# Optimization experiments

Measured on AMD Instinct MI355X. Metric: run time of the kernel, lower is better.

The kernel has to match this reference:

```python
import jax, jax.numpy as jnp
import numpy as np

B, L, D = 16, 196, 512
M = 4096            # existing memory slots
DIS_MEM_LEN = 4096  # M+1 > DIS_MEM_LEN -> eviction always triggers (static shapes)


def setup_inputs() -> dict:
    key = jax.random.key(0)
    ks = jax.random.split(key, 10)
    x = jax.random.normal(ks[0], (B, L, D), jnp.float32)
    feat_mem = jax.random.normal(ks[1], (B, M, D), jnp.float32)
    # freq >= 6 so rm_mask = (freq > 5) is guaranteed nonempty (matches torch
    # branch `if rm_mask.sum() > 0`) and asserts freq != 0, min <= freq hold.
    freq_mem = 6 + jax.random.randint(ks[2], (B, M), 0, 50, jnp.int32)
    min_mem = jax.random.randint(ks[3], (B, M), 0, 6, jnp.int32)
    s = float(1.0 / np.sqrt(D))
    Wv = jax.random.uniform(ks[4], (D, D), jnp.float32, -s, s)
    bv = jax.random.uniform(ks[5], (D,), jnp.float32, -s, s)
    Wu = jax.random.uniform(ks[6], (D, D), jnp.float32, -s, s)
    bu = jax.random.uniform(ks[7], (D,), jnp.float32, -s, s)
    Ww = jax.random.uniform(ks[8], (D, 1), jnp.float32, -s, s)
    bw = jax.random.uniform(ks[9], (1,), jnp.float32, -s, s)
    return dict(x=x, feat_mem=feat_mem, freq_mem=freq_mem, min_mem=min_mem,
                Wv=Wv, bv=bv, Wu=Wu, bu=bu, Ww=Ww, bw=bw)


def reference(x, feat_mem, freq_mem, min_mem, Wv, bv, Wu, bu, Ww, bw):
    bs = x.shape[0]
    cls = x[:, :1, :]                                  # [B, 1, D]
    feat = jnp.concatenate([feat_mem, cls], axis=1)    # [B, M+1, D]
    zero = jnp.zeros((bs, 1), jnp.int32)
    freq = jnp.concatenate([freq_mem, zero], axis=1)   # [B, M+1]
    mn = jnp.concatenate([min_mem, zero], axis=1)      # [B, M+1]

    # gated attention score: sigmoid(Linear(tanh(Lv x) * sigmoid(Lu x)))
    attn_v = jnp.tanh(feat @ Wv + bv)
    attn_u = jax.nn.sigmoid(feat @ Wu + bu)
    attn_score = jax.nn.sigmoid((attn_v * attn_u) @ Ww + bw)  # [B, M+1, 1]

    # eval-mode cur_iter_mask = ones; feat is detached in z in the original
    z = jnp.sum(attn_score * jax.lax.stop_gradient(feat), axis=1)  # [B, D]

    # update_freq_mem: mask is all ones -> +1 everywhere
    freq = freq + 1
    # update_min_mem: argmin of attn_score along memory dim, scatter +1
    attn_idx = jnp.argmin(attn_score[..., 0], axis=1)  # [B]
    mn = mn.at[jnp.arange(bs), attn_idx].add(1)

    # eviction: M+1 > dis_mem_len, remove argmax(min/freq * (freq>5)) per batch
    rm_mask = freq > 5
    ratio = mn.astype(jnp.float32) / freq.astype(jnp.float32) * rm_mask
    rm_idx = jnp.argmax(ratio, axis=1)                 # [B]
    col = jnp.arange(freq.shape[1])[None, :]
    is_rm = col == rm_idx[:, None]                     # [B, M+1] one True per row
    # stable argsort puts kept indices first (in original order), removed one last
    order = jnp.argsort(is_rm, axis=1, stable=True)[:, : freq.shape[1] - 1]
    feat_out = jnp.take_along_axis(feat, order[..., None], axis=1)  # [B, M, D]
    freq_out = jnp.take_along_axis(freq, order, axis=1)             # [B, M]
    min_out = jnp.take_along_axis(mn, order, axis=1)                # [B, M]
    return z, feat_out, freq_out, min_out
```

## Files before the change

kernel.cpp:

```cpp
#include <hip/hip_runtime.h>
#include <cmath>

#define NB 16
#define MM 4096
#define MP1 4097
#define DD 512
#define LSEQ 196
#define NRB 65
#define PSH (32 * 16 * 512)
#define MARGIN 0.05f
#define CANDMAX 128

typedef float f32x4 __attribute__((ext_vector_type(4)));
typedef short bf16x8 __attribute__((ext_vector_type(8)));
typedef unsigned short u16x8 __attribute__((ext_vector_type(8)));

static __device__ __forceinline__ unsigned short bf16_rne(float x) {
  union { float f; unsigned u; } c; c.f = x;
  unsigned u = c.u;
  u += 0x7fffu + ((u >> 16) & 1u);
  return (unsigned short)(u >> 16);
}
static __device__ __forceinline__ float sig_prec(float v) { return 1.0f / (1.0f + expf(-v)); }
static __device__ __forceinline__ float sig_fast(float v) { return 1.0f / (1.0f + __expf(-v)); }
static __device__ __forceinline__ float tanh_fast(float v) { return fmaf(2.0f, sig_fast(2.0f * v), -1.0f); }

__global__ __launch_bounds__(256) void k_packW(const float* __restrict__ Wv,
                                               const float* __restrict__ Wu,
                                               unsigned short* __restrict__ Bp) {
  const int gid = blockIdx.x * 256 + threadIdx.x;
  const int l = gid & 63;
  const int ksg = (gid >> 6) & 15;
  const int ctg = (gid >> 10) & 31;
  const int mat = gid >> 15;
  const float* W = mat ? Wu : Wv;
  const int col = ctg * 16 + (l & 15);
  const int kb = ksg * 32 + (l >> 4) * 8;
  u16x8 hi;
#pragma unroll
  for (int i = 0; i < 8; ++i) hi[i] = bf16_rne(W[(size_t)(kb + i) * DD + col]);
  *(u16x8*)(Bp + (size_t)mat * PSH + ((size_t)(ctg * 16 + ksg)) * 512 + l * 8) = hi;
}

__global__ __launch_bounds__(256) void k_packA(const float* __restrict__ x,
                                               const float* __restrict__ feat_mem,
                                               unsigned short* __restrict__ Ah) {
  const int b = blockIdx.y, rb = blockIdx.x;
  const int kc = threadIdx.x >> 6, l = threadIdx.x & 63;
  unsigned short* dst = Ah + (((size_t)b * NRB + rb) * 4 + kc) * 8192;
#pragma unroll
  for (int f = 0; f < 16; ++f) {
    const int ks = f >> 2, rt = f & 3;
    const int grow = rb * 64 + rt * 16 + (l & 15);
    const int k = kc * 128 + ks * 32 + (l >> 4) * 8;
    float v[8] = {0.f, 0.f, 0.f, 0.f, 0.f, 0.f, 0.f, 0.f};
    if (grow <= MM) {
      const float* src = (grow < MM) ? feat_mem + ((size_t)b * MM + grow) * DD + k
                                     : x + (size_t)b * LSEQ * DD + k;
      const float4 t0 = ((const float4*)src)[0];
      const float4 t1 = ((const float4*)src)[1];
      v[0] = t0.x; v[1] = t0.y; v[2] = t0.z; v[3] = t0.w;
      v[4] = t1.x; v[5] = t1.y; v[6] = t1.z; v[7] = t1.w;
    }
    u16x8 hi;
#pragma unroll
    for (int i = 0; i < 8; ++i) hi[i] = bf16_rne(v[i]);
    *(u16x8*)(dst + f * 512 + l * 8) = hi;
  }
}

__global__ __launch_bounds__(256, 3) void k_scores(
    const unsigned short* __restrict__ Ah, const unsigned short* __restrict__ Bp,
    const float* __restrict__ bv, const float* __restrict__ bu,
    const float* __restrict__ Ww, float* __restrict__ logits) {
  const int rb = blockIdx.x, colb = blockIdx.y, b = blockIdx.z;
  const int tid = threadIdx.x, wave = tid >> 6, l = tid & 63;
  __shared__ __align__(16) unsigned short Alds[2][8192];
  __shared__ float sred[4][64];

  const unsigned short* Abase = Ah + (((size_t)b * NRB + rb) * 4) * 8192;

  f32x4 accv[4][2], accu[4][2];
#pragma unroll
  for (int i = 0; i < 4; ++i)
#pragma unroll
    for (int j = 0; j < 2; ++j) {
      accv[i][j] = (f32x4){0.f, 0.f, 0.f, 0.f};
      accu[i][j] = (f32x4){0.f, 0.f, 0.f, 0.f};
    }

#define STAGE(kc, buf)                                                              \
  {                                                                                 \
    _Pragma("unroll")                                                               \
    for (int r = 0; r < 4; ++r) {                                                   \
      const unsigned short* g = Abase + (kc) * 8192 + r * 2048 + tid * 8;           \
      __builtin_amdgcn_global_load_lds(                                             \
          (const __attribute__((address_space(1))) void*)g,                         \
          (__attribute__((address_space(3))) void*)&Alds[(buf)][r * 2048 + tid * 8],\
          16, 0, 0);                                                                \
    }                                                                               \
  }

  STAGE(0, 0);
  __syncthreads();
  for (int kc = 0; kc < 4; ++kc) {
    if (kc < 3) STAGE(kc + 1, (kc + 1) & 1);
    const unsigned short* Ab = Alds[kc & 1];
#pragma unroll
    for (int ks = 0; ks < 4; ++ks) {
      bf16x8 hiA[4];
#pragma unroll
      for (int rt = 0; rt < 4; ++rt)
        hiA[rt] = *(const bf16x8*)(Ab + (ks * 4 + rt) * 512 + l * 8);
      const int ksg = kc * 4 + ks;
#pragma unroll
      for (int ct = 0; ct < 2; ++ct) {
        const int ctg = colb * 8 + wave * 2 + ct;
        const unsigned short* fb = Bp + ((size_t)(ctg * 16 + ksg)) * 512 + l * 8;
        const bf16x8 hv = *(const bf16x8*)fb;
        const bf16x8 hu = *(const bf16x8*)(fb + PSH);
#pragma unroll
        for (int rt = 0; rt < 4; ++rt) {
          accv[rt][ct] = __builtin_amdgcn_mfma_f32_16x16x32_bf16(hiA[rt], hv, accv[rt][ct], 0, 0, 0);
          accu[rt][ct] = __builtin_amdgcn_mfma_f32_16x16x32_bf16(hiA[rt], hu, accu[rt][ct], 0, 0, 0);
        }
      }
    }
    __syncthreads();
  }
#undef STAGE

  float prow[4][4];
#pragma unroll
  for (int i = 0; i < 4; ++i)
#pragma unroll
    for (int j = 0; j < 4; ++j) prow[i][j] = 0.f;
#pragma unroll
  for (int ct = 0; ct < 2; ++ct) {
    const int col = colb * 128 + wave * 32 + ct * 16 + (l & 15);
    const float bvc = bv[col], buc = bu[col], wwc = Ww[col];
#pragma unroll
    for (int rt = 0; rt < 4; ++rt)
#pragma unroll
      for (int r = 0; r < 4; ++r) {
        const float vv = tanh_fast(accv[rt][ct][r] + bvc);
        const float uu = sig_fast(accu[rt][ct][r] + buc);
        prow[rt][r] = fmaf(vv * uu, wwc, prow[rt][r]);
      }
  }
#pragma unroll
  for (int off = 1; off < 16; off <<= 1)
#pragma unroll
    for (int rt = 0; rt < 4; ++rt)
#pragma unroll
      for (int r = 0; r < 4; ++r) prow[rt][r] += __shfl_xor(prow[rt][r], off, 64);

  if ((l & 15) == 0) {
#pragma unroll
    for (int rt = 0; rt < 4; ++rt)
#pragma unroll
      for (int r = 0; r < 4; ++r) sred[wave][rt * 16 + (l >> 4) * 4 + r] = prow[rt][r];
  }
  __syncthreads();
  if (tid < 64) {
    const float s = sred[0][tid] + sred[1][tid] + sred[2][tid] + sred[3][tid];
    const int row = rb * 64 + tid;
    if (row < MP1) atomicAdd(&logits[(size_t)b * MP1 + row], s);
  }
}

__global__ __launch_bounds__(256) void k_z(const float* __restrict__ x,
                                           const float* __restrict__ feat_mem,
                                           const float* __restrict__ logits,
                                           const float* __restrict__ bw,
                                           float* __restrict__ zacc) {
  const int b = blockIdx.y;
  const int rc = blockIdx.x >> 2;
  const int dc = blockIdx.x & 3;
  const int t = threadIdx.x;
  const int rpar = t >> 5;
  const int d = dc * 128 + (t & 31) * 4;
  const int rbeg = rc * 512;
  const int rend = (rc == 7) ? MP1 : rc * 512 + 512;
  const float bw0 = bw[0];
  float4 acc = make_float4(0.f, 0.f, 0.f, 0.f);
  for (int r = rbeg + rpar; r < rend; r += 8) {
    const float s = sig_fast(logits[(size_t)b * MP1 + r] + bw0);
    const float* src = (r < MM) ? feat_mem + ((size_t)b * MM + r) * DD
                                : x + (size_t)b * LSEQ * DD;
    const float4 f = *(const float4*)(src + d);
    acc.x = fmaf(s, f.x, acc.x);
    acc.y = fmaf(s, f.y, acc.y);
    acc.z = fmaf(s, f.z, acc.z);
    acc.w = fmaf(s, f.w, acc.w);
  }
  __shared__ float4 red[256];
  red[t] = acc;
  __syncthreads();
  if (t < 32) {
    float4 s = red[t];
#pragma unroll
    for (int j = 1; j < 8; ++j) {
      const float4 o = red[t + 32 * j];
      s.x += o.x; s.y += o.y; s.z += o.z; s.w += o.w;
    }
    atomicAdd(&zacc[(size_t)b * DD + d + 0], s.x);
    atomicAdd(&zacc[(size_t)b * DD + d + 1], s.y);
    atomicAdd(&zacc[(size_t)b * DD + d + 2], s.z);
    atomicAdd(&zacc[(size_t)b * DD + d + 3], s.w);
  }
}

__global__ __launch_bounds__(256) void k_cand(const float* __restrict__ logits,
                                              int* __restrict__ cand,
                                              int* __restrict__ cnt) {
  const int b = blockIdx.x, tid = threadIdx.x;
  __shared__ float sv[256];
  __shared__ int scnt;
  float m = INFINITY;
  for (int i = tid; i < MP1; i += 256) m = fminf(m, logits[(size_t)b * MP1 + i]);
  sv[tid] = m;
  __syncthreads();
  for (int s = 128; s >= 1; s >>= 1) {
    if (tid < s) sv[tid] = fminf(sv[tid], sv[tid + s]);
    __syncthreads();
  }
  const float minv = sv[0];
  if (tid == 0) scnt = 0;
  __syncthreads();
  for (int i = tid; i < MP1; i += 256) {
    if (logits[(size_t)b * MP1 + i] <= minv + MARGIN) {
      const int p = atomicAdd(&scnt, 1);
      if (p < CANDMAX) cand[b * CANDMAX + p] = i;
    }
  }
  __syncthreads();
  if (tid == 0) cnt[b] = (scnt < CANDMAX) ? scnt : CANDMAX;
}

__global__ __launch_bounds__(256) void k_refine(
    const float* __restrict__ x, const float* __restrict__ feat_mem,
    const float* __restrict__ Wv, const float* __restrict__ bv,
    const float* __restrict__ Wu, const float* __restrict__ bu,
    const float* __restrict__ Ww,
    const int* __restrict__ cand, const int* __restrict__ cnt,
    float* __restrict__ candpart) {
  const int b = blockIdx.z, c = blockIdx.y, cb = blockIdx.x;
  if (c >= cnt[b]) return;
  const int row = cand[b * CANDMAX + c];
  const int tid = threadIdx.x;
  const int jl = tid & 63;
  const int ks = tid >> 6;
  const int col = cb * 64 + jl;
  __shared__ __align__(16) float sfeat[DD];
  __shared__ float sredv[4][64];
  __shared__ float sredu[4][64];
  const float* src = (row < MM) ? feat_mem + ((size_t)b * MM + row) * DD
                                : x + (size_t)b * LSEQ * DD;
  if (tid < 128) ((float4*)sfeat)[tid] = ((const float4*)src)[tid];
  __syncthreads();
  float v = 0.f, u = 0.f;
  const float* wvp = Wv + (size_t)(ks * 128) * DD + col;
  const float* wup = Wu + (size_t)(ks * 128) * DD + col;
#pragma unroll 8
  for (int k = 0; k < 128; ++k) {
    const float a = sfeat[ks * 128 + k];
    v = fmaf(a, wvp[(size_t)k * DD], v);
    u = fmaf(a, wup[(size_t)k * DD], u);
  }
  sredv[ks][jl] = v;
  sredu[ks][jl] = u;
  __syncthreads();
  if (tid < 64) {
    const float vv = (sredv[0][jl] + sredv[1][jl]) + (sredv[2][jl] + sredv[3][jl]);
    const float uu = (sredu[0][jl] + sredu[1][jl]) + (sredu[2][jl] + sredu[3][jl]);
    float g = tanhf(vv + bv[col]) * sig_prec(uu + bu[col]) * Ww[col];
#pragma unroll
    for (int off = 1; off < 64; off <<= 1) g += __shfl_xor(g, off, 64);
    if (jl == 0) candpart[((size_t)b * CANDMAX + c) * 8 + cb] = g;
  }
}

__global__ __launch_bounds__(256) void k_finalize2(
    const int* __restrict__ cand, const float* __restrict__ candpart,
    const int* __restrict__ cnt, const int* __restrict__ freq_mem,
    const int* __restrict__ min_mem, const float* __restrict__ zacc,
    float* __restrict__ out_z, float* __restrict__ out_freq,
    float* __restrict__ out_min, int* __restrict__ rm_attn) {
  const int b = blockIdx.x, tid = threadIdx.x;
  __shared__ float sv[256];
  __shared__ int si[256];
  __shared__ int sn[256], sd[256], sj[256];
  __shared__ int s_attn, s_rm;

  const int n = cnt[b];
  float v = INFINITY;
  int idx = MP1;
  if (tid < n) {
    const float* p = candpart + ((size_t)b * CANDMAX + tid) * 8;
    v = ((p[0] + p[1]) + (p[2] + p[3])) + ((p[4] + p[5]) + (p[6] + p[7]));
    idx = cand[b * CANDMAX + tid];
  }
  sv[tid] = v; si[tid] = idx;
  __syncthreads();
  for (int s = 128; s >= 1; s >>= 1) {
    if (tid < s) {
      const float v2 = sv[tid + s]; const int i2 = si[tid + s];
      if (v2 < sv[tid] || (v2 == sv[tid] && i2 < si[tid])) { sv[tid] = v2; si[tid] = i2; }
    }
    __syncthreads();
  }
  if (tid == 0) s_attn = si[0];
  __syncthreads();
  const int attn = s_attn;

  int bn = -1, bd = 1, bj = 0;
  for (int i = tid; i < MP1; i += 256) {
    int num, den;
    if (i < MM) {
      den = freq_mem[(size_t)b * MM + i] + 1;
      num = min_mem[(size_t)b * MM + i] + (i == attn ? 1 : 0);
      if (den <= 5) num = 0;
    } else { den = 1; num = 0; }
    if (num * bd > bn * den) { bn = num; bd = den; bj = i; }
  }
  sn[tid] = bn; sd[tid] = bd; sj[tid] = bj;
  __syncthreads();
  for (int s = 128; s >= 1; s >>= 1) {
    if (tid < s) {
      const int n2 = sn[tid + s], d2 = sd[tid + s], j2 = sj[tid + s];
      const int lft = n2 * sd[tid], rgt = sn[tid] * d2;
      if (lft > rgt || (lft == rgt && j2 < sj[tid])) { sn[tid] = n2; sd[tid] = d2; sj[tid] = j2; }
    }
    __syncthreads();
  }
  if (tid == 0) { s_rm = sj[0]; rm_attn[b * 2] = attn; rm_attn[b * 2 + 1] = sj[0]; }
  __syncthreads();
  const int rm = s_rm;

  for (int i = tid; i < MM; i += 256) {
    const int src = (i < rm) ? i : i + 1;
    int fv, mv;
    if (src < MM) {
      fv = freq_mem[(size_t)b * MM + src] + 1;
      mv = min_mem[(size_t)b * MM + src] + (src == attn ? 1 : 0);
    } else {
      fv = 1; mv = (attn == MM) ? 1 : 0;
    }
    out_freq[(size_t)b * MM + i] = (float)fv;
    out_min[(size_t)b * MM + i] = (float)mv;
  }
  for (int d = tid; d < DD; d += 256) out_z[(size_t)b * DD + d] = zacc[(size_t)b * DD + d];
}

__global__ __launch_bounds__(256) void k_gather(
    const float* __restrict__ feat_mem, const float* __restrict__ x,
    const int* __restrict__ rm_attn, float* __restrict__ out_feat) {
  const int b = blockIdx.y;
  const int rm = rm_attn[b * 2 + 1];
  const int row = blockIdx.x * 4 + (threadIdx.x >> 6);
  const int lane = threadIdx.x & 63;
  const int src = (row < rm) ? row : row + 1;
  const float* sp = (src < MM) ? (feat_mem + ((size_t)b * MM + src) * DD)
                               : (x + (size_t)b * LSEQ * DD);
  float* dp = out_feat + ((size_t)b * MM + row) * DD;
  const float4 v0 = reinterpret_cast<const float4*>(sp)[lane];
  const float4 v1 = reinterpret_cast<const float4*>(sp)[lane + 64];
  reinterpret_cast<float4*>(dp)[lane] = v0;
  reinterpret_cast<float4*>(dp)[lane + 64] = v1;
}

extern "C" void kernel_launch(void* const* d_in, const int* in_sizes, int n_in,
                              void* d_out, int out_size, void* d_ws, size_t ws_size,
                              hipStream_t stream) {
  const float* x        = (const float*)d_in[0];
  const float* feat_mem = (const float*)d_in[1];
  const int*   freq_mem = (const int*)d_in[2];
  const int*   min_mem  = (const int*)d_in[3];
  const float* Wv       = (const float*)d_in[4];
  const float* bv       = (const float*)d_in[5];
  const float* Wu       = (const float*)d_in[6];
  const float* bu       = (const float*)d_in[7];
  const float* Ww       = (const float*)d_in[8];
  const float* bw       = (const float*)d_in[9];

  float* ws       = (float*)d_ws;
  float* logits   = ws;
  float* zacc     = ws + NB * MP1;
  float* candpart = zacc + NB * DD;
  int*   cand     = (int*)(candpart + NB * CANDMAX * 8);
  int*   cnt      = cand + NB * CANDMAX;
  int*   rm_attn  = cnt + NB;
  unsigned short* Bp = (unsigned short*)(rm_attn + 32);

  float* out_z    = (float*)d_out;
  float* out_feat = out_z + NB * DD;
  float* out_freq = out_feat + (size_t)NB * MM * DD;
  float* out_min  = out_freq + (size_t)NB * MM;

  unsigned short* Ah = (unsigned short*)out_feat;

  hipMemsetAsync(logits, 0, (NB * MP1 + NB * DD) * sizeof(float), stream);
  hipMemsetAsync(cnt, 0, NB * sizeof(int), stream);

  k_packW<<<dim3(256), dim3(256), 0, stream>>>(Wv, Wu, Bp);
  k_packA<<<dim3(NRB, NB), dim3(256), 0, stream>>>(x, feat_mem, Ah);
  k_scores<<<dim3(NRB, 4, NB), dim3(256), 0, stream>>>(Ah, Bp, bv, bu, Ww, logits);
  k_z<<<dim3(32, NB), dim3(256), 0, stream>>>(x, feat_mem, logits, bw, zacc);
  k_cand<<<dim3(NB), dim3(256), 0, stream>>>(logits, cand, cnt);
  k_refine<<<dim3(8, CANDMAX, NB), dim3(256), 0, stream>>>(x, feat_mem, Wv, bv, Wu, bu, Ww,
                                                           cand, cnt, candpart);
  k_finalize2<<<dim3(NB), dim3(256), 0, stream>>>(cand, candpart, cnt, freq_mem, min_mem, zacc,
                                                  out_z, out_freq, out_min, rm_attn);
  k_gather<<<dim3(MM / 4, NB), dim3(256), 0, stream>>>(feat_mem, x, rm_attn, out_feat);
}
```

Measured before the change: 263.3 us.

## Fuse fp32-to-bf16 activation packing into the scores GEMM kernel

Removes the separate k_packA pass that converted feat_mem to a bf16 staging buffer. The scores kernel now loads fp32 rows directly, converts them with packed bf16 conversion instructions, and writes them into double-buffered LDS while the MFMAs for the previous K chunk run. Blocks grow to 512 threads covering 256 output columns, and Wv/Wu tiles are interleaved so each wave reads consecutive tiles. This avoids writing and re-reading the bf16 copy of the memory bank, but each block now reads twice as many bytes of fp32 A data (which is re-read by both column blocks), and register pressure rises.

After: 334.7 us. +27.1%, slower.

```diff
diff --git a/kernel.cpp b/kernel.cpp
--- a/kernel.cpp
+++ b/kernel.cpp
@@ -7,7 +7,6 @@
 #define DD 512
 #define LSEQ 196
 #define NRB 65
-#define PSH (32 * 16 * 512)
 #define MARGIN 0.05f
 #define CANDMAX 128
 
@@ -21,13 +20,18 @@
   u += 0x7fffu + ((u >> 16) & 1u);
   return (unsigned short)(u >> 16);
 }
+static __device__ __forceinline__ unsigned cvt_pk_bf16(float lo, float hi) {
+  unsigned r;
+  asm("v_cvt_pk_bf16_f32 %0, %1, %2" : "=v"(r) : "v"(lo), "v"(hi));
+  return r;
+}
 static __device__ __forceinline__ float sig_prec(float v) { return 1.0f / (1.0f + expf(-v)); }
 static __device__ __forceinline__ float sig_fast(float v) { return 1.0f / (1.0f + __expf(-v)); }
 static __device__ __forceinline__ float tanh_fast(float v) { return fmaf(2.0f, sig_fast(2.0f * v), -1.0f); }
 
 __global__ __launch_bounds__(256) void k_packW(const float* __restrict__ Wv,
                                                const float* __restrict__ Wu,
-                                               unsigned short* __restrict__ Bp) {
+                                               unsigned short* __restrict__ Bc) {
   const int gid = blockIdx.x * 256 + threadIdx.x;
   const int l = gid & 63;
   const int ksg = (gid >> 6) & 15;
@@ -39,72 +43,74 @@
   u16x8 hi;
 #pragma unroll
   for (int i = 0; i < 8; ++i) hi[i] = bf16_rne(W[(size_t)(kb + i) * DD + col]);
-  *(u16x8*)(Bp + (size_t)mat * PSH + ((size_t)(ctg * 16 + ksg)) * 512 + l * 8) = hi;
-}
-
-__global__ __launch_bounds__(256) void k_packA(const float* __restrict__ x,
-                                               const float* __restrict__ feat_mem,
-                                               unsigned short* __restrict__ Ah) {
-  const int b = blockIdx.y, rb = blockIdx.x;
-  const int kc = threadIdx.x >> 6, l = threadIdx.x & 63;
-  unsigned short* dst = Ah + (((size_t)b * NRB + rb) * 4 + kc) * 8192;
-#pragma unroll
-  for (int f = 0; f < 16; ++f) {
-    const int ks = f >> 2, rt = f & 3;
-    const int grow = rb * 64 + rt * 16 + (l & 15);
-    const int k = kc * 128 + ks * 32 + (l >> 4) * 8;
-    float v[8] = {0.f, 0.f, 0.f, 0.f, 0.f, 0.f, 0.f, 0.f};
-    if (grow <= MM) {
-      const float* src = (grow < MM) ? feat_mem + ((size_t)b * MM + grow) * DD + k
-                                     : x + (size_t)b * LSEQ * DD + k;
-      const float4 t0 = ((const float4*)src)[0];
-      const float4 t1 = ((const float4*)src)[1];
-      v[0] = t0.x; v[1] = t0.y; v[2] = t0.z; v[3] = t0.w;
-      v[4] = t1.x; v[5] = t1.y; v[6] = t1.z; v[7] = t1.w;
-    }
-    u16x8 hi;
-#pragma unroll
-    for (int i = 0; i < 8; ++i) hi[i] = bf16_rne(v[i]);
-    *(u16x8*)(dst + f * 512 + l * 8) = hi;
-  }
-}
-
-__global__ __launch_bounds__(256, 3) void k_scores(
-    const unsigned short* __restrict__ Ah, const unsigned short* __restrict__ Bp,
+  const int ctg2 = ctg * 2 + mat;
+  *(u16x8*)(Bc + ((size_t)(ctg2 * 16 + ksg)) * 512 + l * 8) = hi;
+}
+
+__global__ __launch_bounds__(512, 2) void k_scores(
+    const float* __restrict__ x, const float* __restrict__ feat_mem,
+    const unsigned short* __restrict__ Bc,
     const float* __restrict__ bv, const float* __restrict__ bu,
     const float* __restrict__ Ww, float* __restrict__ logits) {
-  const int rb = blockIdx.x, colb = blockIdx.y, b = blockIdx.z;
+  const int colb = blockIdx.x, rb = blockIdx.y, b = blockIdx.z;
+  const int row0 = rb * 64;
   const int tid = threadIdx.x, wave = tid >> 6, l = tid & 63;
+
   __shared__ __align__(16) unsigned short Alds[2][8192];
-  __shared__ float sred[4][64];
-
-  const unsigned short* Abase = Ah + (((size_t)b * NRB + rb) * 4) * 8192;
-
-  f32x4 accv[4][2], accu[4][2];
+  __shared__ float sred[8][64];
+
+  f32x4 acc[4][4];
 #pragma unroll
   for (int i = 0; i < 4; ++i)
 #pragma unroll
-    for (int j = 0; j < 2; ++j) {
-      accv[i][j] = (f32x4){0.f, 0.f, 0.f, 0.f};
-      accu[i][j] = (f32x4){0.f, 0.f, 0.f, 0.f};
-    }
-
-#define STAGE(kc, buf)                                                              \
-  {                                                                                 \
-    _Pragma("unroll")                                                               \
-    for (int r = 0; r < 4; ++r) {                                                   \
-      const unsigned short* g = Abase + (kc) * 8192 + r * 2048 + tid * 8;           \
-      __builtin_amdgcn_global_load_lds(                                             \
-          (const __attribute__((address_space(1))) void*)g,                         \
-          (__attribute__((address_space(3))) void*)&Alds[(buf)][r * 2048 + tid * 8],\
-          16, 0, 0);                                                                \
-    }                                                                               \
-  }
-
-  STAGE(0, 0);
-  __syncthreads();
+    for (int j = 0; j < 4; ++j) acc[i][j] = (f32x4){0.f, 0.f, 0.f, 0.f};
+
+  const int fa = tid >> 6;
+  const int srow = (fa & 3) * 16 + (l & 15);
+  const int grow = row0 + srow;
+  const int kA = ((fa >> 2) * 32) + ((l >> 4) * 8);
+  const float* srcrow = nullptr;
+  if (grow < MM) srcrow = feat_mem + ((size_t)b * MM + grow) * DD;
+  else if (grow == MM) srcrow = x + (size_t)b * LSEQ * DD;
+  const int woffA = fa * 512 + l * 8;
+  const int woffB = (fa + 8) * 512 + l * 8;
+
+  float4 a0, a1, a2, a3;
+#define LOADK(kc)                                                     \
+  {                                                                   \
+    if (srcrow) {                                                     \
+      const float* p = srcrow + (kc) * 128 + kA;                      \
+      a0 = ((const float4*)p)[0];                                     \
+      a1 = ((const float4*)(p + 4))[0];                               \
+      a2 = ((const float4*)(p + 64))[0];                              \
+      a3 = ((const float4*)(p + 68))[0];                              \
+    } else {                                                          \
+      a0 = a1 = a2 = a3 = make_float4(0.f, 0.f, 0.f, 0.f);            \
+    }                                                                 \
+  }
+#define WRITEK(buf)                                                   \
+  {                                                                   \
+    union { unsigned u[4]; u16x8 v; } pA, pB;                         \
+    pA.u[0] = cvt_pk_bf16(a0.x, a0.y);                                \
+    pA.u[1] = cvt_pk_bf16(a0.z, a0.w);                                \
+    pA.u[2] = cvt_pk_bf16(a1.x, a1.y);                                \
+    pA.u[3] = cvt_pk_bf16(a1.z, a1.w);                                \
+    pB.u[0] = cvt_pk_bf16(a2.x, a2.y);                                \
+    pB.u[1] = cvt_pk_bf16(a2.z, a2.w);                                \
+    pB.u[2] = cvt_pk_bf16(a3.x, a3.y);                                \
+    pB.u[3] = cvt_pk_bf16(a3.z, a3.w);                                \
+    *(u16x8*)(Alds[(buf)] + woffA) = pA.v;                            \
+    *(u16x8*)(Alds[(buf)] + woffB) = pB.v;                            \
+  }
+
+  LOADK(0);
+  WRITEK(0);
+  __syncthreads();
+
+  const unsigned short* Bwave = Bc + ((size_t)(colb * 32 + wave * 4) * 16) * 512 + l * 8;
+
   for (int kc = 0; kc < 4; ++kc) {
-    if (kc < 3) STAGE(kc + 1, (kc + 1) & 1);
+    if (kc < 3) LOADK(kc + 1);
     const unsigned short* Ab = Alds[kc & 1];
 #pragma unroll
     for (int ks = 0; ks < 4; ++ks) {
@@ -114,21 +120,18 @@
         hiA[rt] = *(const bf16x8*)(Ab + (ks * 4 + rt) * 512 + l * 8);
       const int ksg = kc * 4 + ks;
 #pragma unroll
-      for (int ct = 0; ct < 2; ++ct) {
-        const int ctg = colb * 8 + wave * 2 + ct;
-        const unsigned short* fb = Bp + ((size_t)(ctg * 16 + ksg)) * 512 + l * 8;
-        const bf16x8 hv = *(const bf16x8*)fb;
-        const bf16x8 hu = *(const bf16x8*)(fb + PSH);
-#pragma unroll
-        for (int rt = 0; rt < 4; ++rt) {
-          accv[rt][ct] = __builtin_amdgcn_mfma_f32_16x16x32_bf16(hiA[rt], hv, accv[rt][ct], 0, 0, 0);
-          accu[rt][ct] = __builtin_amdgcn_mfma_f32_16x16x32_bf16(hiA[rt], hu, accu[rt][ct], 0, 0, 0);
-        }
+      for (int ct = 0; ct < 4; ++ct) {
+        const bf16x8 bb = *(const bf16x8*)(Bwave + (size_t)(ct * 16 + ksg) * 512);
+#pragma unroll
+        for (int rt = 0; rt < 4; ++rt)
+          acc[rt][ct] = __builtin_amdgcn_mfma_f32_16x16x32_bf16(hiA[rt], bb, acc[rt][ct], 0, 0, 0);
       }
     }
+    if (kc < 3) WRITEK((kc + 1) & 1);
     __syncthreads();
   }
-#undef STAGE
+#undef LOADK
+#undef WRITEK
 
   float prow[4][4];
 #pragma unroll
@@ -136,15 +139,15 @@
 #pragma unroll
     for (int j = 0; j < 4; ++j) prow[i][j] = 0.f;
 #pragma unroll
-  for (int ct = 0; ct < 2; ++ct) {
-    const int col = colb * 128 + wave * 32 + ct * 16 + (l & 15);
+  for (int gp = 0; gp < 2; ++gp) {
+    const int col = (colb * 16 + wave * 2 + gp) * 16 + (l & 15);
     const float bvc = bv[col], buc = bu[col], wwc = Ww[col];
 #pragma unroll
     for (int rt = 0; rt < 4; ++rt)
 #pragma unroll
       for (int r = 0; r < 4; ++r) {
-        const float vv = tanh_fast(accv[rt][ct][r] + bvc);
-        const float uu = sig_fast(accu[rt][ct][r] + buc);
+        const float vv = tanh_fast(acc[rt][2 * gp][r] + bvc);
+        const float uu = sig_fast(acc[rt][2 * gp + 1][r] + buc);
         prow[rt][r] = fmaf(vv * uu, wwc, prow[rt][r]);
       }
   }
@@ -163,8 +166,10 @@
   }
   __syncthreads();
   if (tid < 64) {
-    const float s = sred[0][tid] + sred[1][tid] + sred[2][tid] + sred[3][tid];
-    const int row = rb * 64 + tid;
+    float s = 0.f;
+#pragma unroll
+    for (int w = 0; w < 8; ++w) s += sred[w][tid];
+    const int row = row0 + tid;
     if (row < MP1) atomicAdd(&logits[(size_t)b * MP1 + row], s);
   }
 }
@@ -391,21 +396,18 @@
   int*   cand     = (int*)(candpart + NB * CANDMAX * 8);
   int*   cnt      = cand + NB * CANDMAX;
   int*   rm_attn  = cnt + NB;
-  unsigned short* Bp = (unsigned short*)(rm_attn + 32);
+  unsigned short* Bc = (unsigned short*)(rm_attn + 32);
 
   float* out_z    = (float*)d_out;
   float* out_feat = out_z + NB * DD;
   float* out_freq = out_feat + (size_t)NB * MM * DD;
   float* out_min  = out_freq + (size_t)NB * MM;
 
-  unsigned short* Ah = (unsigned short*)out_feat;
-
   hipMemsetAsync(logits, 0, (NB * MP1 + NB * DD) * sizeof(float), stream);
   hipMemsetAsync(cnt, 0, NB * sizeof(int), stream);
 
-  k_packW<<<dim3(256), dim3(256), 0, stream>>>(Wv, Wu, Bp);
-  k_packA<<<dim3(NRB, NB), dim3(256), 0, stream>>>(x, feat_mem, Ah);
-  k_scores<<<dim3(NRB, 4, NB), dim3(256), 0, stream>>>(Ah, Bp, bv, bu, Ww, logits);
+  k_packW<<<dim3(256), dim3(256), 0, stream>>>(Wv, Wu, Bc);
+  k_scores<<<dim3(2, NRB, NB), dim3(512), 0, stream>>>(x, feat_mem, Bc, bv, bu, Ww, logits);
   k_z<<<dim3(32, NB), dim3(256), 0, stream>>>(x, feat_mem, logits, bw, zacc);
   k_cand<<<dim3(NB), dim3(256), 0, stream>>>(logits, cand, cnt);
   k_refine<<<dim3(8, CANDMAX, NB), dim3(256), 0, stream>>>(x, feat_mem, Wv, bv, Wu, bu, Ww,
```
